# Optimization experiments

Hardware: AMD Instinct MI355X
Metric: run time of the kernel (lower is better)

Reference implementation:

```python
import jax, jax.numpy as jnp
import numpy as np

B, L1, L2, D1, D2 = 32, 2048, 2048, 1024, 1024


def setup_inputs() -> dict:
    key = jax.random.key(0)
    k1, k2, k3 = jax.random.split(key, 3)
    x1 = jax.random.normal(k1, (B, L1, D1), dtype=jnp.float32)
    x2 = jax.random.normal(k2, (B, L2, D2), dtype=jnp.float32)
    # xavier_normal_ init for U [dim1, dim2]
    std = float(np.sqrt(2.0 / (D1 + D2)))
    U = jax.random.normal(k3, (D1, D2), dtype=jnp.float32) * std
    return {"x1": x1, "x2": x2, "U": U}


def reference(x1, x2, U):
    # M[b,i,j] = x1[b,i,:] @ U @ x2[b,j,:]  -> [B, L1, L2]
    M = jnp.einsum('bid,de,bje->bij', x1, U, x2)
    # row attention: max over L2 then softmax over L1 -> [B, L1]
    rows = jax.nn.softmax(M.max(axis=2), axis=1)
    # col attention: max over L1 then softmax over L2 -> [B, L2]
    cols = jax.nn.softmax(M.max(axis=1), axis=1)
    _x1 = jnp.einsum('bi,bid->bd', rows, x1)  # [B, D1]
    _x2 = jnp.einsum('bj,bjd->bd', cols, x2)  # [B, D2]
    return (_x1, _x2)
```

## Files before the change

### kernel.cpp

```cpp
#include <hip/hip_runtime.h>
#include <hip/hip_bf16.h>
#include <stdint.h>

#define B_  32
#define L_  2048
#define D_  1024

typedef __attribute__((ext_vector_type(8))) _Float16 f16x8;
typedef __attribute__((ext_vector_type(4))) float f32x4;

__device__ __forceinline__ unsigned enc_f(float x) {
  unsigned u = __float_as_uint(x);
  return (u & 0x80000000u) ? ~u : (u | 0x80000000u);
}
__device__ __forceinline__ float dec_f(unsigned e) {
  unsigned u = (e & 0x80000000u) ? (e ^ 0x80000000u) : ~e;
  return __uint_as_float(u);
}
__device__ __forceinline__ ushort f16_bits(float x) {
  _Float16 h = (_Float16)x;
  return __builtin_bit_cast(ushort, h);
}
__device__ __forceinline__ void split_f16(float x, ushort& h, ushort& l) {
  _Float16 hf = (_Float16)x;
  float r = x - (float)hf;
  h = __builtin_bit_cast(ushort, hf);
  l = __builtin_bit_cast(ushort, (_Float16)r);
}

__device__ __forceinline__ void gl_lds16(const ushort* g, ushort* l) {
  using gas_t = const __attribute__((address_space(1))) uint32_t*;
  using las_t = __attribute__((address_space(3))) uint32_t*;
  __builtin_amdgcn_global_load_lds((gas_t)(uintptr_t)g,
                                   (las_t)(unsigned)(uintptr_t)l, 16, 0, 0);
}

__global__ void dec1_k(const float4* __restrict__ x, uint2* __restrict__ h, int n4) {
  int i = blockIdx.x * blockDim.x + threadIdx.x;
  const int stride = gridDim.x * blockDim.x;
  for (; i < n4; i += stride) {
    float4 v = x[i];
    uint2 hw;
    hw.x = (unsigned)f16_bits(v.x) | ((unsigned)f16_bits(v.y) << 16);
    hw.y = (unsigned)f16_bits(v.z) | ((unsigned)f16_bits(v.w) << 16);
    h[i] = hw;
  }
}

__global__ void transdec_k(const float* __restrict__ U,
                           ushort* __restrict__ UTh, ushort* __restrict__ UTl) {
  __shared__ float t[32][33];
  const int tx = threadIdx.x, ty = threadIdx.y;
  const int e0 = blockIdx.x * 32, d0 = blockIdx.y * 32;
#pragma unroll
  for (int r = 0; r < 4; ++r)
    t[ty + r * 8][tx] = U[(size_t)(d0 + ty + r * 8) * D_ + e0 + tx];
  __syncthreads();
#pragma unroll
  for (int r = 0; r < 4; ++r) {
    int e = ty + r * 8;
    ushort h, l;
    split_f16(t[tx][e] * 2048.0f, h, l);
    UTh[(size_t)(e0 + e) * D_ + d0 + tx] = h;
    UTl[(size_t)(e0 + e) * D_ + d0 + tx] = l;
  }
}

struct CoreCtx {
  int w, lane, ln, kq, wm, wn, ko;
  size_t soA;
};

__device__ __forceinline__ CoreCtx make_ctx() {
  CoreCtx c;
  const int tid = threadIdx.x;
  c.w = tid >> 6; c.lane = tid & 63;
  c.ln = c.lane & 15; c.kq = c.lane >> 4;
  c.wm = c.w >> 2; c.wn = c.w & 3;
  c.ko = (c.kq ^ ((c.ln >> 1) & 3)) * 8;
  const int srow = c.lane >> 2;
  const int sslot = (c.lane & 3) ^ ((c.lane >> 3) & 3);
  c.soA = (size_t)(c.w * 32 + srow) * D_ + sslot * 8;
  return c;
}

__device__ __forceinline__ void stage_plane(const ushort* src, ushort* dstbase,
                                            const CoreCtx& c, int k0) {
  const size_t a0 = c.soA + k0, a1 = a0 + (size_t)16 * D_;
  ushort* d0 = dstbase + c.w * 1024;
  gl_lds16(src + a0, d0);
  gl_lds16(src + a1, d0 + 512);
}

#define VMCNT(n) asm volatile("s_waitcnt vmcnt(" #n ")" ::: "memory")
#define BARRIER() do { asm volatile("" ::: "memory"); \
                       __builtin_amdgcn_s_barrier();  \
                       asm volatile("" ::: "memory"); } while (0)

__device__ __forceinline__ void core_loop3(const CoreCtx& c,
    const ushort* Ah, const ushort* Bh, const ushort* Bl,
    ushort* lbuf, f32x4 acc[8][4])
{
  stage_plane(Ah, lbuf,         c, 0);
  stage_plane(Bh, lbuf + 8192,  c, 0);
  stage_plane(Bl, lbuf + 16384, c, 0);

  for (int t = 0; t < 32; ++t) {
    const ushort* cb = lbuf + (t & 1) * 24576;
    ushort* nb = lbuf + ((t + 1) & 1) * 24576;
    const int kn = (t + 1) * 32;
    const bool pf = (t < 31);
    f16x8 a[8], bh4[4], bl4[4];

    VMCNT(2);
    BARRIER();
#pragma unroll
    for (int n = 0; n < 4; ++n) {
      const int r = c.wn * 64 + n * 16 + c.ln;
      bh4[n] = *(const f16x8*)&cb[8192 + r * 32 + c.ko];
    }
#pragma unroll
    for (int m = 0; m < 8; ++m) {
      const int r = c.wm * 128 + m * 16 + c.ln;
      a[m] = *(const f16x8*)&cb[r * 32 + c.ko];
    }
    if (pf) { stage_plane(Ah, nb, c, kn); stage_plane(Bh, nb + 8192, c, kn); }
    __builtin_amdgcn_s_setprio(1);
#pragma unroll
    for (int m = 0; m < 8; ++m)
#pragma unroll
      for (int n = 0; n < 4; ++n)
        acc[m][n] = __builtin_amdgcn_mfma_f32_16x16x32_f16(a[m], bh4[n], acc[m][n], 0, 0, 0);
    __builtin_amdgcn_s_setprio(0);

    if (pf) { VMCNT(4); } else { VMCNT(0); }
    BARRIER();
#pragma unroll
    for (int n = 0; n < 4; ++n) {
      const int r = c.wn * 64 + n * 16 + c.ln;
      bl4[n] = *(const f16x8*)&cb[16384 + r * 32 + c.ko];
    }
    if (pf) stage_plane(Bl, nb + 16384, c, kn);
    __builtin_amdgcn_s_setprio(1);
#pragma unroll
    for (int m = 0; m < 8; ++m)
#pragma unroll
      for (int n = 0; n < 4; ++n)
        acc[m][n] = __builtin_amdgcn_mfma_f32_16x16x32_f16(a[m], bl4[n], acc[m][n], 0, 0, 0);
    __builtin_amdgcn_s_setprio(0);
  }
}

__global__ __launch_bounds__(512, 2) void gemm1_k(
    const ushort* __restrict__ x1h,
    const ushort* __restrict__ UTh, const ushort* __restrict__ UTl,
    ushort* __restrict__ Yh)
{
  __shared__ __attribute__((aligned(16))) ushort lbuf[65536];
  const int z = blockIdx.z;
  const int orig = blockIdx.x;
  const int xc = orig & 7, j = orig >> 3;
  const int bx = (xc & 3) * 2 + (j & 1);
  const int by = (xc >> 2) * 2 + (j >> 1);

  const size_t zb = (size_t)z * (L_ * D_);
  const ushort* Ah = x1h + zb + (size_t)bx * 256 * D_;
  const ushort* Bh = UTh + (size_t)by * 256 * D_;
  const ushort* Bl = UTl + (size_t)by * 256 * D_;

  CoreCtx c = make_ctx();
  f32x4 acc[8][4];
#pragma unroll
  for (int m = 0; m < 8; ++m)
#pragma unroll
    for (int n = 0; n < 4; ++n) acc[m][n] = (f32x4){0.f, 0.f, 0.f, 0.f};

  core_loop3(c, Ah, Bh, Bl, lbuf, acc);

  __syncthreads();

  ushort* ep = lbuf + c.w * 8192;
  const int grow = bx * 256 + c.wm * 128;
  const int gcol = by * 256 + c.wn * 64;
#pragma unroll
  for (int m = 0; m < 8; ++m)
#pragma unroll
    for (int n = 0; n < 4; ++n)
#pragma unroll
      for (int r2 = 0; r2 < 4; ++r2) {
        float v = acc[m][n][r2] * 4.8828125e-4f;
        ep[(m * 16 + c.kq * 4 + r2) * 64 + n * 16 + c.ln] = f16_bits(v);
      }
#pragma unroll
  for (int q = 0; q < 16; ++q) {
    const int chunk = q * 64 + c.lane;
    const int row = chunk >> 3, c8 = (chunk & 7) * 8;
    f16x8 v = *(const f16x8*)&ep[row * 64 + c8];
    *(f16x8*)&Yh[zb + (size_t)(grow + row) * D_ + gcol + c8] = v;
  }
}

__global__ __launch_bounds__(512, 2) void gemm2_k(
    const ushort* __restrict__ Yh,
    const ushort* __restrict__ x2h,
    unsigned* __restrict__ rmxg, unsigned* __restrict__ cmxg)
{
  __shared__ __attribute__((aligned(16))) ushort lbuf[65536];
  const int z = blockIdx.z;
  const int orig = blockIdx.x;
  const int xc = orig & 7, j = orig >> 3;
  const int bx = (xc & 3) * 2 + (j & 1);
  const int by = (xc >> 2) * 4 + (j >> 1);

  const size_t zb = (size_t)z * (L_ * D_);
  const ushort* Ap = Yh + zb + (size_t)bx * 256 * D_;
  const ushort* Bp = x2h + zb + (size_t)by * 256 * D_;

  const int tid = threadIdx.x;
  const int w = tid >> 6, lane = tid & 63;
  const int ln = lane & 15, kq = lane >> 4;
  const int wm = w >> 2, wn = w & 3;
  const int ko0 = ((kq)     ^ (ln & 7)) * 8;
  const int ko1 = ((4 + kq) ^ (ln & 7)) * 8;
  const int srow8 = lane >> 3;
  const int sslot8 = (lane & 7) ^ srow8;
  const size_t sOff = (size_t)(w * 16 + srow8) * D_ + sslot8 * 8;

  f32x4 acc[8][4];
#pragma unroll
  for (int m = 0; m < 8; ++m)
#pragma unroll
    for (int n = 0; n < 4; ++n) acc[m][n] = (f32x4){0.f, 0.f, 0.f, 0.f};

  const ushort* srcH0 = Ap;
  const ushort* srcH1 = Ap + (size_t)128 * D_;
  const ushort* srcH2 = Bp;
  const ushort* srcH3 = Bp + (size_t)128 * D_;

#define STAGE_H(nb, hbase, srcp, kt)                                   \
  do {                                                                 \
    const size_t a_ = sOff + (size_t)(kt) * 64;                        \
    ushort* d_ = (nb) + (hbase) + w * 1024;                            \
    gl_lds16((srcp) + a_, d_);                                         \
    gl_lds16((srcp) + a_ + (size_t)8 * D_, d_ + 512);                  \
  } while (0)

  STAGE_H(lbuf, 0,     srcH0, 0);
  STAGE_H(lbuf, 8192,  srcH1, 0);
  STAGE_H(lbuf, 16384, srcH2, 0);
  STAGE_H(lbuf, 24576, srcH3, 0);
  VMCNT(0);
  BARRIER();

  for (int t = 0; t < 16; ++t) {
    const ushort* cb = lbuf + (t & 1) * 32768;
    ushort* nb = lbuf + ((t + 1) & 1) * 32768;
    const bool pf = (t < 15);
    const int kn = t + 1;
    const ushort* aB = cb + wm * 8192;
    const ushort* bB = cb + 16384 + (wn >> 1) * 8192;
    const int rB = (wn & 1) * 64;

    f16x8 aX[4], aY[4], b0[4], b1[4];

#pragma unroll
    for (int n = 0; n < 4; ++n)
      b0[n] = *(const f16x8*)&bB[(rB + n * 16 + ln) * 64 + ko0];
#pragma unroll
    for (int m = 0; m < 4; ++m)
      aX[m] = *(const f16x8*)&aB[(m * 16 + ln) * 64 + ko0];
    if (pf) STAGE_H(nb, 0, srcH0, kn);
    __builtin_amdgcn_s_setprio(1);
#pragma unroll
    for (int m = 0; m < 4; ++m)
#pragma unroll
      for (int n = 0; n < 4; ++n)
        acc[m][n] = __builtin_amdgcn_mfma_f32_16x16x32_f16(aX[m], b0[n], acc[m][n], 0, 0, 0);
    __builtin_amdgcn_s_setprio(0);
    __builtin_amdgcn_sched_barrier(0);

#pragma unroll
    for (int m = 0; m < 4; ++m)
      aY[m] = *(const f16x8*)&aB[((64 + m * 16 + ln)) * 64 + ko0];
    if (pf) STAGE_H(nb, 8192, srcH1, kn);
    __builtin_amdgcn_s_setprio(1);
#pragma unroll
    for (int m = 0; m < 4; ++m)
#pragma unroll
      for (int n = 0; n < 4; ++n)
        acc[4 + m][n] = __builtin_amdgcn_mfma_f32_16x16x32_f16(aY[m], b0[n], acc[4 + m][n], 0, 0, 0);
    __builtin_amdgcn_s_setprio(0);
    __builtin_amdgcn_sched_barrier(0);

#pragma unroll
    for (int n = 0; n < 4; ++n)
      b1[n] = *(const f16x8*)&bB[(rB + n * 16 + ln) * 64 + ko1];
#pragma unroll
    for (int m = 0; m < 4; ++m)
      aX[m] = *(const f16x8*)&aB[(m * 16 + ln) * 64 + ko1];
    if (pf) { STAGE_H(nb, 16384, srcH2, kn); STAGE_H(nb, 24576, srcH3, kn); }
    __builtin_amdgcn_s_setprio(1);
#pragma unroll
    for (int m = 0; m < 4; ++m)
#pragma unroll
      for (int n = 0; n < 4; ++n)
        acc[m][n] = __builtin_amdgcn_mfma_f32_16x16x32_f16(aX[m], b1[n], acc[m][n], 0, 0, 0);
    __builtin_amdgcn_s_setprio(0);
    __builtin_amdgcn_sched_barrier(0);

#pragma unroll
    for (int m = 0; m < 4; ++m)
      aY[m] = *(const f16x8*)&aB[((64 + m * 16 + ln)) * 64 + ko1];
    __builtin_amdgcn_s_setprio(1);
#pragma unroll
    for (int m = 0; m < 4; ++m)
#pragma unroll
      for (int n = 0; n < 4; ++n)
        acc[4 + m][n] = __builtin_amdgcn_mfma_f32_16x16x32_f16(aY[m], b1[n], acc[4 + m][n], 0, 0, 0);
    __builtin_amdgcn_s_setprio(0);

    if (pf) { VMCNT(0); }
    BARRIER();
  }

  __syncthreads();
  unsigned* red = (unsigned*)lbuf;
  red[tid] = 0u;
  __syncthreads();

#pragma unroll
  for (int m = 0; m < 8; ++m) {
#pragma unroll
    for (int r2 = 0; r2 < 4; ++r2) {
      float v = fmaxf(fmaxf(acc[m][0][r2], acc[m][1][r2]),
                      fmaxf(acc[m][2][r2], acc[m][3][r2]));
#pragma unroll
      for (int s = 1; s < 16; s <<= 1) v = fmaxf(v, __shfl_xor(v, s));
      if (ln == 0) atomicMax(&red[wm * 128 + m * 16 + kq * 4 + r2], enc_f(v));
    }
  }
#pragma unroll
  for (int n = 0; n < 4; ++n) {
    float v = -3.4e38f;
#pragma unroll
    for (int m = 0; m < 8; ++m)
#pragma unroll
      for (int r2 = 0; r2 < 4; ++r2) v = fmaxf(v, acc[m][n][r2]);
    v = fmaxf(v, __shfl_xor(v, 16));
    v = fmaxf(v, __shfl_xor(v, 32));
    if (kq == 0) atomicMax(&red[256 + wn * 64 + n * 16 + ln], enc_f(v));
  }
  __syncthreads();
  if (tid < 256) atomicMax(&rmxg[(size_t)z * L_ + bx * 256 + tid], red[tid]);
  else           atomicMax(&cmxg[(size_t)z * L_ + by * 256 + (tid - 256)], red[tid]);
#undef STAGE_H
}

__global__ void softmax_k(const unsigned* __restrict__ enc, float* __restrict__ w) {
  __shared__ float red[256];
  const int b = blockIdx.x, tid = threadIdx.x;
  const unsigned* e = enc + (size_t)b * L_;
  float* wb = w + (size_t)b * L_;
  float vals[8];
  float lmax = -3.4e38f;
#pragma unroll
  for (int q = 0; q < 8; ++q) {
    float f = dec_f(e[q * 256 + tid]);
    vals[q] = f;
    lmax = fmaxf(lmax, f);
  }
  red[tid] = lmax; __syncthreads();
  for (int s = 128; s > 0; s >>= 1) {
    if (tid < s) red[tid] = fmaxf(red[tid], red[tid + s]);
    __syncthreads();
  }
  const float mx = red[0];
  __syncthreads();
  float lsum = 0.f;
#pragma unroll
  for (int q = 0; q < 8; ++q) { vals[q] = expf(vals[q] - mx); lsum += vals[q]; }
  red[tid] = lsum; __syncthreads();
  for (int s = 128; s > 0; s >>= 1) {
    if (tid < s) red[tid] += red[tid + s];
    __syncthreads();
  }
  const float inv = 1.f / red[0];
#pragma unroll
  for (int q = 0; q < 8; ++q) wb[q * 256 + tid] = vals[q] * inv;
}

__global__ void wsum_k(const float* __restrict__ w, const ushort* __restrict__ xh,
                       float* __restrict__ out) {
  __shared__ float ws[256];
  const int tid = threadIdx.x;
  const int b = blockIdx.y;
  const int i0 = blockIdx.x * 256;
  ws[tid] = w[(size_t)b * L_ + i0 + tid];
  __syncthreads();
  const int d0 = tid * 4;
  const ushort* xb = xh + ((size_t)b * L_ + i0) * D_ + d0;
  float4 acc = {0.f, 0.f, 0.f, 0.f};
  for (int i = 0; i < 256; ++i) {
    ushort4 v = *(const ushort4*)(xb + (size_t)i * D_);
    float wi = ws[i];
    acc.x = fmaf(wi, (float)__builtin_bit_cast(_Float16, v.x), acc.x);
    acc.y = fmaf(wi, (float)__builtin_bit_cast(_Float16, v.y), acc.y);
    acc.z = fmaf(wi, (float)__builtin_bit_cast(_Float16, v.z), acc.z);
    acc.w = fmaf(wi, (float)__builtin_bit_cast(_Float16, v.w), acc.w);
  }
  float* o = out + (size_t)b * D_ + d0;
  atomicAdd(o + 0, acc.x);
  atomicAdd(o + 1, acc.y);
  atomicAdd(o + 2, acc.z);
  atomicAdd(o + 3, acc.w);
}

extern "C" void kernel_launch(void* const* d_in, const int* in_sizes, int n_in,
                              void* d_out, int out_size, void* d_ws, size_t ws_size,
                              hipStream_t stream) {
  (void)in_sizes; (void)n_in; (void)out_size;
  const float* x1 = (const float*)d_in[0];
  const float* x2 = (const float*)d_in[1];
  const float* U  = (const float*)d_in[2];
  float* out = (float*)d_out;

  char* p = (char*)d_ws;
  ushort* UTh = (ushort*)p; p += (size_t)D_ * D_ * 2;
  ushort* UTl = (ushort*)p; p += (size_t)D_ * D_ * 2;
  unsigned* rowmax = (unsigned*)p; p += (size_t)B_ * L_ * 4;
  unsigned* colmax = (unsigned*)p; p += (size_t)B_ * L_ * 4;
  float* w1 = (float*)p; p += (size_t)B_ * L_ * 4;
  float* w2 = (float*)p; p += (size_t)B_ * L_ * 4;
  const size_t fixed = (size_t)(p - (char*)d_ws);
  const size_t perB = (size_t)3 * L_ * D_ * 2;
  int G = 1;
  if (ws_size > fixed) {
    size_t g = (ws_size - fixed) / perB;
    G = g < 1 ? 1 : (g > (size_t)B_ ? B_ : (int)g);
  }
  ushort* x1h = (ushort*)p;
  ushort* x2h = x1h + (size_t)G * L_ * D_;
  ushort* Yh  = x2h + (size_t)G * L_ * D_;

  hipMemsetAsync(d_out, 0, (size_t)2 * B_ * D_ * 4, stream);
  hipMemsetAsync(rowmax, 0, (size_t)2 * B_ * L_ * 4, stream);

  transdec_k<<<dim3(32, 32), dim3(32, 8), 0, stream>>>(U, UTh, UTl);

  for (int g0 = 0; g0 < B_; g0 += G) {
    const int Gc = (B_ - g0) < G ? (B_ - g0) : G;
    const int n4 = Gc * (L_ * D_ / 4);
    dec1_k<<<dim3(1024), 256, 0, stream>>>(
        (const float4*)(x1 + (size_t)g0 * L_ * D_), (uint2*)x1h, n4);
    dec1_k<<<dim3(1024), 256, 0, stream>>>(
        (const float4*)(x2 + (size_t)g0 * L_ * D_), (uint2*)x2h, n4);
    gemm1_k<<<dim3(32, 1, Gc), 512, 0, stream>>>(x1h, UTh, UTl, Yh);
    gemm2_k<<<dim3(64, 1, Gc), 512, 0, stream>>>(Yh, x2h,
        rowmax + (size_t)g0 * L_, colmax + (size_t)g0 * L_);
    softmax_k<<<dim3(Gc), 256, 0, stream>>>(rowmax + (size_t)g0 * L_,
                                            w1 + (size_t)g0 * L_);
    softmax_k<<<dim3(Gc), 256, 0, stream>>>(colmax + (size_t)g0 * L_,
                                            w2 + (size_t)g0 * L_);
    wsum_k<<<dim3(8, Gc), 256, 0, stream>>>(w1 + (size_t)g0 * L_, x1h,
                                            out + (size_t)g0 * D_);
    wsum_k<<<dim3(8, Gc), 256, 0, stream>>>(w2 + (size_t)g0 * L_, x2h,
                                            out + (size_t)(B_ + g0) * D_);
  }
}
```

Before: 720.5 us.

## Split GEMM K-step into four quarter-tile phases with fine-grained vmcnt waits

Restructures the main fp16 MFMA loop of the bilinear-score kernel. Global-to-LDS staging is split into four quarter tiles (A first/second half, B first/second half), and each quarter feeds one 4x2 MFMA sub-block. Partial vmcnt waits let compute start on the quarter that has landed while the others are still in flight, replacing the single full drain at the end of each K step. The aim is to hide load latency and shorten the exposed prefetch wait. The cost is several extra workgroup barriers per iteration, plus more complex wait-count bookkeeping that must stay correct across the double buffer.

```diff
diff --git a/kernel.cpp b/kernel.cpp
--- a/kernel.cpp
+++ b/kernel.cpp
@@ -222,9 +222,10 @@
   const int wm = w >> 2, wn = w & 3;
   const int ko0 = ((kq)     ^ (ln & 7)) * 8;
   const int ko1 = ((4 + kq) ^ (ln & 7)) * 8;
-  const int srow8 = lane >> 3;
-  const int sslot8 = (lane & 7) ^ srow8;
-  const size_t sOff = (size_t)(w * 16 + srow8) * D_ + sslot8 * 8;
+  const int srh = lane >> 3;
+  const int ssl = (lane & 7) ^ srh;
+  const int rA0 = (w >> 2) * 128 + (w & 3) * 16;
+  const int rB0 = (w >> 1) * 64 + (w & 1) * 16;
 
   f32x4 acc[8][4];
 #pragma unroll
@@ -232,96 +233,110 @@
 #pragma unroll
     for (int n = 0; n < 4; ++n) acc[m][n] = (f32x4){0.f, 0.f, 0.f, 0.f};
 
-  const ushort* srcH0 = Ap;
-  const ushort* srcH1 = Ap + (size_t)128 * D_;
-  const ushort* srcH2 = Bp;
-  const ushort* srcH3 = Bp + (size_t)128 * D_;
-
-#define STAGE_H(nb, hbase, srcp, kt)                                   \
-  do {                                                                 \
-    const size_t a_ = sOff + (size_t)(kt) * 64;                        \
-    ushort* d_ = (nb) + (hbase) + w * 1024;                            \
-    gl_lds16((srcp) + a_, d_);                                         \
-    gl_lds16((srcp) + a_ + (size_t)8 * D_, d_ + 512);                  \
+#define STG(nbuf, plofs, srcp, rowbase, kt) do {                                     \
+    const size_t a_ = (size_t)((rowbase) + srh) * D_ + (size_t)(kt) * 64 + ssl * 8;  \
+    ushort* d_ = (nbuf) + (plofs) + (rowbase) * 64;                                  \
+    gl_lds16((srcp) + a_, d_);                                                       \
+    gl_lds16((srcp) + a_ + (size_t)8 * D_, d_ + 512);                                \
   } while (0)
 
-  STAGE_H(lbuf, 0,     srcH0, 0);
-  STAGE_H(lbuf, 8192,  srcH1, 0);
-  STAGE_H(lbuf, 16384, srcH2, 0);
-  STAGE_H(lbuf, 24576, srcH3, 0);
-  VMCNT(0);
+  STG(lbuf, 0,     Ap, rA0,      0);
+  STG(lbuf, 16384, Bp, rB0,      0);
+  STG(lbuf, 16384, Bp, rB0 + 32, 0);
+  STG(lbuf, 0,     Ap, rA0 + 64, 0);
+  VMCNT(4);
   BARRIER();
+
+  f16x8 a[4][2], b0[2][2], b1[2][2];
 
   for (int t = 0; t < 16; ++t) {
     const ushort* cb = lbuf + (t & 1) * 32768;
     ushort* nb = lbuf + ((t + 1) & 1) * 32768;
     const bool pf = (t < 15);
     const int kn = t + 1;
-    const ushort* aB = cb + wm * 8192;
-    const ushort* bB = cb + 16384 + (wn >> 1) * 8192;
-    const int rB = (wn & 1) * 64;
-
-    f16x8 aX[4], aY[4], b0[4], b1[4];
-
-#pragma unroll
-    for (int n = 0; n < 4; ++n)
-      b0[n] = *(const f16x8*)&bB[(rB + n * 16 + ln) * 64 + ko0];
-#pragma unroll
-    for (int m = 0; m < 4; ++m)
-      aX[m] = *(const f16x8*)&aB[(m * 16 + ln) * 64 + ko0];
-    if (pf) STAGE_H(nb, 0, srcH0, kn);
-    __builtin_amdgcn_s_setprio(1);
-#pragma unroll
-    for (int m = 0; m < 4; ++m)
-#pragma unroll
-      for (int n = 0; n < 4; ++n)
-        acc[m][n] = __builtin_amdgcn_mfma_f32_16x16x32_f16(aX[m], b0[n], acc[m][n], 0, 0, 0);
-    __builtin_amdgcn_s_setprio(0);
-    __builtin_amdgcn_sched_barrier(0);
-
-#pragma unroll
-    for (int m = 0; m < 4; ++m)
-      aY[m] = *(const f16x8*)&aB[((64 + m * 16 + ln)) * 64 + ko0];
-    if (pf) STAGE_H(nb, 8192, srcH1, kn);
-    __builtin_amdgcn_s_setprio(1);
-#pragma unroll
-    for (int m = 0; m < 4; ++m)
-#pragma unroll
-      for (int n = 0; n < 4; ++n)
-        acc[4 + m][n] = __builtin_amdgcn_mfma_f32_16x16x32_f16(aY[m], b0[n], acc[4 + m][n], 0, 0, 0);
-    __builtin_amdgcn_s_setprio(0);
-    __builtin_amdgcn_sched_barrier(0);
-
-#pragma unroll
-    for (int n = 0; n < 4; ++n)
-      b1[n] = *(const f16x8*)&bB[(rB + n * 16 + ln) * 64 + ko1];
-#pragma unroll
-    for (int m = 0; m < 4; ++m)
-      aX[m] = *(const f16x8*)&aB[(m * 16 + ln) * 64 + ko1];
-    if (pf) { STAGE_H(nb, 16384, srcH2, kn); STAGE_H(nb, 24576, srcH3, kn); }
-    __builtin_amdgcn_s_setprio(1);
-#pragma unroll
-    for (int m = 0; m < 4; ++m)
-#pragma unroll
-      for (int n = 0; n < 4; ++n)
-        acc[m][n] = __builtin_amdgcn_mfma_f32_16x16x32_f16(aX[m], b1[n], acc[m][n], 0, 0, 0);
-    __builtin_amdgcn_s_setprio(0);
-    __builtin_amdgcn_sched_barrier(0);
-
-#pragma unroll
-    for (int m = 0; m < 4; ++m)
-      aY[m] = *(const f16x8*)&aB[((64 + m * 16 + ln)) * 64 + ko1];
-    __builtin_amdgcn_s_setprio(1);
-#pragma unroll
-    for (int m = 0; m < 4; ++m)
-#pragma unroll
-      for (int n = 0; n < 4; ++n)
-        acc[4 + m][n] = __builtin_amdgcn_mfma_f32_16x16x32_f16(aY[m], b1[n], acc[4 + m][n], 0, 0, 0);
-    __builtin_amdgcn_s_setprio(0);
-
-    if (pf) { VMCNT(0); }
-    BARRIER();
-  }
+    const ushort* aP = cb;
+    const ushort* bP = cb + 16384;
+
+#pragma unroll
+    for (int ks = 0; ks < 2; ++ks) {
+      const int ko = ks ? ko1 : ko0;
+#pragma unroll
+      for (int nt = 0; nt < 2; ++nt)
+        b0[nt][ks] = *(const f16x8*)&bP[(wn * 64 + nt * 16 + ln) * 64 + ko];
+#pragma unroll
+      for (int m = 0; m < 4; ++m)
+        a[m][ks] = *(const f16x8*)&aP[(wm * 128 + m * 16 + ln) * 64 + ko];
+    }
+    if (pf) STG(nb, 0, Ap, rA0, kn);
+    if (pf) { VMCNT(4); } else { VMCNT(2); }
+    BARRIER();
+    __builtin_amdgcn_s_setprio(1);
+#pragma unroll
+    for (int ks = 0; ks < 2; ++ks)
+#pragma unroll
+      for (int m = 0; m < 4; ++m)
+#pragma unroll
+        for (int nt = 0; nt < 2; ++nt)
+          acc[m][nt] = __builtin_amdgcn_mfma_f32_16x16x32_f16(a[m][ks], b0[nt][ks], acc[m][nt], 0, 0, 0);
+    __builtin_amdgcn_s_setprio(0);
+    BARRIER();
+
+#pragma unroll
+    for (int ks = 0; ks < 2; ++ks) {
+      const int ko = ks ? ko1 : ko0;
+#pragma unroll
+      for (int nt = 0; nt < 2; ++nt)
+        b1[nt][ks] = *(const f16x8*)&bP[(wn * 64 + (2 + nt) * 16 + ln) * 64 + ko];
+    }
+    if (pf) STG(nb, 16384, Bp, rB0, kn);
+    if (pf) { VMCNT(4); } else { VMCNT(0); }
+    BARRIER();
+    __builtin_amdgcn_s_setprio(1);
+#pragma unroll
+    for (int ks = 0; ks < 2; ++ks)
+#pragma unroll
+      for (int m = 0; m < 4; ++m)
+#pragma unroll
+        for (int nt = 0; nt < 2; ++nt)
+          acc[m][2 + nt] = __builtin_amdgcn_mfma_f32_16x16x32_f16(a[m][ks], b1[nt][ks], acc[m][2 + nt], 0, 0, 0);
+    __builtin_amdgcn_s_setprio(0);
+    BARRIER();
+
+#pragma unroll
+    for (int ks = 0; ks < 2; ++ks) {
+      const int ko = ks ? ko1 : ko0;
+#pragma unroll
+      for (int m = 0; m < 4; ++m)
+        a[m][ks] = *(const f16x8*)&aP[(wm * 128 + (4 + m) * 16 + ln) * 64 + ko];
+    }
+    if (pf) STG(nb, 16384, Bp, rB0 + 32, kn);
+    BARRIER();
+    __builtin_amdgcn_s_setprio(1);
+#pragma unroll
+    for (int ks = 0; ks < 2; ++ks)
+#pragma unroll
+      for (int m = 0; m < 4; ++m)
+#pragma unroll
+        for (int nt = 0; nt < 2; ++nt)
+          acc[4 + m][nt] = __builtin_amdgcn_mfma_f32_16x16x32_f16(a[m][ks], b0[nt][ks], acc[4 + m][nt], 0, 0, 0);
+    __builtin_amdgcn_s_setprio(0);
+    BARRIER();
+
+    if (pf) STG(nb, 0, Ap, rA0 + 64, kn);
+    if (pf) { VMCNT(4); }
+    BARRIER();
+    __builtin_amdgcn_s_setprio(1);
+#pragma unroll
+    for (int ks = 0; ks < 2; ++ks)
+#pragma unroll
+      for (int m = 0; m < 4; ++m)
+#pragma unroll
+        for (int nt = 0; nt < 2; ++nt)
+          acc[4 + m][2 + nt] = __builtin_amdgcn_mfma_f32_16x16x32_f16(a[m][ks], b1[nt][ks], acc[4 + m][2 + nt], 0, 0, 0);
+    __builtin_amdgcn_s_setprio(0);
+    BARRIER();
+  }
+#undef STG
 
   __syncthreads();
   unsigned* red = (unsigned*)lbuf;
@@ -353,7 +368,6 @@
   __syncthreads();
   if (tid < 256) atomicMax(&rmxg[(size_t)z * L_ + bx * 256 + tid], red[tid]);
   else           atomicMax(&cmxg[(size_t)z * L_ + by * 256 + (tid - 256)], red[tid]);
-#undef STAGE_H
 }
 
 __global__ void softmax_k(const unsigned* __restrict__ enc, float* __restrict__ w) {
```

Result: no change. 713.9 us (median of 2 runs) (-0.9%).
